# Kernel tuning notes

Hardware: AMD Instinct MI355X
Metric: run time of the kernel (lower is better)

The kernel has to match this reference:

```python
import jax, jax.numpy as jnp
import numpy as np

NUM_EXPERTS = 8
CAP_FACTOR = 1.0
MIN_CAPACITY = 4


def setup_inputs() -> dict:
    key = jax.random.key(0)
    k0, k1, k2, k3 = jax.random.split(key, 4)
    H, F, E = 2048, 8192, NUM_EXPERTS
    hidden_states = jax.random.normal(k0, (4, 2048, H), dtype=jnp.float32)
    wg = jax.random.normal(k1, (H, E), dtype=jnp.float32) * 0.02
    w1 = jax.random.normal(k2, (E, H, F), dtype=jnp.float32) * 0.02
    b1 = jnp.zeros((E, F), dtype=jnp.float32)
    w2 = jax.random.normal(k3, (E, F, H), dtype=jnp.float32) * 0.02
    b2 = jnp.zeros((E, H), dtype=jnp.float32)
    return {"hidden_states": hidden_states, "wg": wg, "w1": w1, "b1": b1,
            "w2": w2, "b2": b2}


def reference(hidden_states, wg, w1, b1, w2, b2):
    E = NUM_EXPERTS
    M = hidden_states.shape[-1]
    x = hidden_states.reshape(-1, M)                     # [S, M] tokens
    S = x.shape[0]
    capacity = max(int(np.ceil(S / E * CAP_FACTOR)), MIN_CAPACITY)  # static

    # --- top-1 gating (DeepSpeed top1gating, fp32) ---
    logits = x.astype(jnp.float32) @ wg                  # [S, E]
    gates = jax.nn.softmax(logits, axis=-1)              # [S, E]
    idx1 = jnp.argmax(gates, axis=1)                     # [S]
    mask1 = jax.nn.one_hot(idx1, E, dtype=jnp.int32)     # [S, E]

    # load-balancing aux loss and per-expert counts
    me = jnp.mean(gates, axis=0)
    ce = jnp.mean(mask1.astype(jnp.float32), axis=0)
    l_aux = jnp.sum(me * ce) * E
    exp_counts = jnp.sum(mask1, axis=0)                  # [E]

    # capacity enforcement (use_rts=False -> keep earliest tokens per expert)
    locations1 = jnp.cumsum(mask1, axis=0) - 1           # [S, E] slot index
    mask1 = mask1 * (locations1 < capacity).astype(jnp.int32)
    mask1f = mask1.astype(gates.dtype)
    gates = gates * mask1f                               # zero dropped/other experts
    locs_s = jnp.sum(locations1 * mask1, axis=1)         # [S] slot of each token
    locs_sc = jax.nn.one_hot(locs_s, capacity, dtype=gates.dtype)  # [S, C]

    # combine / dispatch tensors
    combine = jnp.einsum('se,sc->sec', gates, locs_sc)   # [S, E, C]
    dispatch = (combine > 0).astype(x.dtype)             # bool mask as float

    # dispatch -> grouped expert MLP -> combine
    dispatched = jnp.einsum('sec,sm->ecm', dispatch, x)  # [E, C, M]
    h = jax.nn.gelu(jnp.einsum('ecm,emf->ecf', dispatched, w1) + b1[:, None, :])
    expert_out = jnp.einsum('ecf,efm->ecm', h, w2) + b2[:, None, :]
    out = jnp.einsum('sec,ecm->sm', combine.astype(x.dtype), expert_out)

    return out.reshape(hidden_states.shape), l_aux, exp_counts
```

## Files before the change

### kernel.cpp

```cpp
#include <hip/hip_runtime.h>
#include <stdint.h>

#define E_ 8
#define S_ 8192
#define H_ 2048
#define F_ 8192
#define C_ 1024
#define OUTN (S_*H_)

typedef __bf16 bf16x8 __attribute__((ext_vector_type(8)));
typedef float  f32x4  __attribute__((ext_vector_type(4)));
typedef unsigned short us8 __attribute__((ext_vector_type(8)));

__device__ __forceinline__ unsigned short f2bf(float f) {
    union { float f; unsigned u; } v; v.f = f;
    unsigned r = (v.u + 0x7FFFu + ((v.u >> 16) & 1u)) >> 16;
    return (unsigned short)r;
}

__device__ __forceinline__ void gload16(const void* g, void* l) {
    auto gp = (const __attribute__((address_space(1))) void*)(unsigned long long)(uintptr_t)g;
    auto lp = (__attribute__((address_space(3))) void*)(unsigned int)(uintptr_t)l;
    __builtin_amdgcn_global_load_lds(gp, lp, 16, 0, 0);
}

#define SB() __builtin_amdgcn_sched_barrier(0)
#define BAR() do { SB(); __builtin_amdgcn_s_barrier(); SB(); } while(0)

__global__ void zero_kernel(float* __restrict__ o, int n) {
    int i = blockIdx.x * blockDim.x + threadIdx.x;
    int st = gridDim.x * blockDim.x;
    for (; i < n; i += st) o[i] = 0.f;
}

__global__ __launch_bounds__(256)
void transpose_cvt(const float* __restrict__ src, unsigned short* __restrict__ dst,
                   int R, int Cc)
{
    __shared__ float t[64][65];
    int tilesR = R >> 6, tilesC = Cc >> 6;
    int per_e = tilesR * tilesC;
    int bid = blockIdx.x;
    int e  = bid / per_e;
    int rm = bid - e * per_e;
    int tc = rm / tilesR;
    int tr = rm - tc * tilesR;

    const float* s = src + (size_t)e * R * Cc + (size_t)(tr * 64) * Cc + tc * 64;
    int tid = threadIdx.x;
    int rr = tid >> 4;
    int cc = (tid & 15) << 2;
#pragma unroll
    for (int i = 0; i < 4; i++) {
        float4 v = *(const float4*)(s + (size_t)(rr + i * 16) * Cc + cc);
        t[rr + i * 16][cc + 0] = v.x;
        t[rr + i * 16][cc + 1] = v.y;
        t[rr + i * 16][cc + 2] = v.z;
        t[rr + i * 16][cc + 3] = v.w;
    }
    __syncthreads();
    int nl = tid >> 2;
    int kq = (tid & 3) << 4;
    us8 o0, o1;
#pragma unroll
    for (int i = 0; i < 8; i++) o0[i] = f2bf(t[kq + i][nl]);
#pragma unroll
    for (int i = 0; i < 8; i++) o1[i] = f2bf(t[kq + 8 + i][nl]);
    unsigned short* d = dst + (size_t)e * R * Cc + (size_t)(tc * 64 + nl) * R + tr * 64 + kq;
    *reinterpret_cast<us8*>(d)     = o0;
    *reinterpret_cast<us8*>(d + 8) = o1;
}

__global__ __launch_bounds__(256)
void gating_kernel(const float* __restrict__ x, const float* __restrict__ wg,
                   int* __restrict__ expert_id, float* __restrict__ gate_tok,
                   float* __restrict__ gates_all)
{
    int lane = threadIdx.x & 63;
    int wid  = threadIdx.x >> 6;
    int s = blockIdx.x * 4 + wid;
    const float* xs = x + (size_t)s * H_;
    float p[8];
#pragma unroll
    for (int j = 0; j < 8; j++) p[j] = 0.f;
    for (int h = lane; h < H_; h += 64) {
        float xv = xs[h];
        const float4* w4 = (const float4*)(wg + (size_t)h * 8);
        float4 a = w4[0], b = w4[1];
        p[0] += xv * a.x; p[1] += xv * a.y; p[2] += xv * a.z; p[3] += xv * a.w;
        p[4] += xv * b.x; p[5] += xv * b.y; p[6] += xv * b.z; p[7] += xv * b.w;
    }
#pragma unroll
    for (int off = 32; off; off >>= 1) {
#pragma unroll
        for (int j = 0; j < 8; j++) p[j] += __shfl_xor(p[j], off);
    }
    if (lane == 0) {
        float mx = p[0];
#pragma unroll
        for (int j = 1; j < 8; j++) mx = fmaxf(mx, p[j]);
        float ex[8], sum = 0.f;
#pragma unroll
        for (int j = 0; j < 8; j++) { ex[j] = expf(p[j] - mx); sum += ex[j]; }
        float inv = 1.f / sum;
        int am = 0; float best = p[0];
#pragma unroll
        for (int j = 1; j < 8; j++) if (p[j] > best) { best = p[j]; am = j; }
        expert_id[s] = am;
        gate_tok[s]  = expf(best - mx) * inv;
        float* ga = gates_all + (size_t)s * 8;
#pragma unroll
        for (int j = 0; j < 8; j++) ga[j] = ex[j] * inv;
    }
}

__global__ __launch_bounds__(1024)
void scan_kernel(const int* __restrict__ expert_id,
                 const float* __restrict__ gate_tok,
                 const float* __restrict__ gates_all,
                 int* __restrict__ token_slot,
                 float* __restrict__ gate_slot,
                 float* __restrict__ out_tail)
{
    __shared__ unsigned long long wt0[16], wt1[16];
    __shared__ unsigned long long tot0s, tot1s;
    __shared__ float red[1024 * 8];

    int tid = threadIdx.x;
    for (int i = tid; i < E_ * C_; i += 1024) token_slot[i] = -1;

    int ids[8];
#pragma unroll
    for (int j = 0; j < 8; j++) ids[j] = expert_id[tid * 8 + j];

    unsigned long long c0 = 0, c1 = 0;
#pragma unroll
    for (int j = 0; j < 8; j++) {
        int e = ids[j];
        unsigned long long inc = 1ull << ((e & 3) * 16);
        if (e < 4) c0 += inc; else c1 += inc;
    }
    unsigned long long s0 = c0, s1 = c1;
    int lane = tid & 63, w = tid >> 6;
#pragma unroll
    for (int off = 1; off < 64; off <<= 1) {
        unsigned long long t0 = __shfl_up(s0, off);
        unsigned long long t1 = __shfl_up(s1, off);
        if (lane >= off) { s0 += t0; s1 += t1; }
    }
    if (lane == 63) { wt0[w] = s0; wt1[w] = s1; }
    __syncthreads();
    unsigned long long off0 = 0, off1 = 0;
    for (int i = 0; i < w; i++) { off0 += wt0[i]; off1 += wt1[i]; }
    unsigned long long p0 = off0 + s0 - c0;
    unsigned long long p1 = off1 + s1 - c1;

#pragma unroll
    for (int j = 0; j < 8; j++) {
        int stok = tid * 8 + j;
        int e = ids[j];
        int sh = (e & 3) * 16;
        int slot = (int)(((e < 4 ? p0 : p1) >> sh) & 0xFFFFull);
        if (slot < C_) {
            token_slot[e * C_ + slot] = stok;
            gate_slot[e * C_ + slot]  = gate_tok[stok];
        }
        if (e < 4) p0 += 1ull << sh; else p1 += 1ull << sh;
    }
    if (tid == 1023) { tot0s = off0 + s0; tot1s = off1 + s1; }

    float me[8];
#pragma unroll
    for (int e2 = 0; e2 < 8; e2++) me[e2] = 0.f;
#pragma unroll
    for (int j = 0; j < 8; j++) {
        const float* ga = gates_all + (size_t)(tid * 8 + j) * 8;
#pragma unroll
        for (int e2 = 0; e2 < 8; e2++) me[e2] += ga[e2];
    }
#pragma unroll
    for (int e2 = 0; e2 < 8; e2++) red[tid * 8 + e2] = me[e2];
    __syncthreads();
    for (int st = 512; st > 0; st >>= 1) {
        if (tid < st) {
#pragma unroll
            for (int e2 = 0; e2 < 8; e2++) red[tid * 8 + e2] += red[(tid + st) * 8 + e2];
        }
        __syncthreads();
    }
    if (tid == 0) {
        float laux = 0.f;
#pragma unroll
        for (int e2 = 0; e2 < 8; e2++) {
            unsigned long long tv = (e2 < 4) ? tot0s : tot1s;
            float cnt = (float)((tv >> ((e2 & 3) * 16)) & 0xFFFFull);
            laux += red[e2] * cnt;
            out_tail[1 + e2] = cnt;
        }
        out_tail[0] = laux * (8.f / (8192.f * 8192.f));
    }
}

__global__ __launch_bounds__(256)
void gather_kernel(const float* __restrict__ x, const int* __restrict__ token_slot,
                   unsigned short* __restrict__ disp)
{
    int slot = blockIdx.x;
    int tok = token_slot[slot];
    int t = threadIdx.x;
    us8* d = reinterpret_cast<us8*>(disp + (size_t)slot * H_ + t * 8);
    if (tok < 0) {
        us8 z;
#pragma unroll
        for (int i = 0; i < 8; i++) z[i] = 0;
        *d = z;
        return;
    }
    const float4* s4 = (const float4*)(x + (size_t)tok * H_ + t * 8);
    float4 a = s4[0], b = s4[1];
    us8 o;
    o[0] = f2bf(a.x); o[1] = f2bf(a.y); o[2] = f2bf(a.z); o[3] = f2bf(a.w);
    o[4] = f2bf(b.x); o[5] = f2bf(b.y); o[6] = f2bf(b.z); o[7] = f2bf(b.w);
    *d = o;
}

template<int EPI, int K, int N>
__global__ __launch_bounds__(512, 2)
void gemm8p(const unsigned short* __restrict__ A,
            const unsigned short* __restrict__ B,
            const float* __restrict__ bias,
            unsigned short* __restrict__ hout,
            float* __restrict__ fout,
            const int* __restrict__ token_slot,
            const float* __restrict__ gate_slot,
            int Mt, int Nt)
{
    __shared__ char lds[131072];
    constexpr int KB   = K * 2;
    constexpr int HALF = 128 * KB;
    constexpr int NTI  = K / 64;

    int nwg = gridDim.x;
    int bid = blockIdx.x;
    int cpx = nwg >> 3;
    int wg  = (bid & 7) * cpx + (bid >> 3);
    int per_e = Mt * Nt;
    int e  = wg / per_e;
    int r  = wg - e * per_e;
    int nt = r / Mt;
    int mt = r - nt * Mt;

    int tid  = threadIdx.x;
    int lane = tid & 63;
    int wid  = tid >> 6;
    int wr = wid >> 2, wc = wid & 3;

    const char* Ag = (const char*)(A + ((size_t)e * 1024 + (size_t)mt * 256) * (size_t)K);
    const char* Bg = (const char*)(B + ((size_t)e * N    + (size_t)nt * 256) * (size_t)K);

    int r16s   = (tid >> 2) & 15;
    int scs    = ((tid & 3) * 16) ^ ((r16s & 8) << 2);
    int colblk = (tid >> 6) & 1;
    int rb0    = tid >> 7;
    int off0 = (rb0 * 16 + r16s) * KB + colblk * 64 + scs;
    int off1 = off0 + 64 * KB;
    int widb = wid * 1024;

    int lread = (lane & 15) * 64 + (((lane >> 4) * 16) ^ ((lane & 8) << 2));

    auto STAGE = [&](int ldsbase, const char* srcbase) {
        gload16(srcbase + off0, (char*)&lds[ldsbase + widb]);
        gload16(srcbase + off1, (char*)&lds[ldsbase + 8192 + widb]);
    };

    STAGE(0,         Ag);
    STAGE(16384,     Ag + HALF);
    STAGE(32768,     Bg);
    STAGE(49152,     Bg + HALF);
    STAGE(65536,     Ag + 128);
    STAGE(65536 + 16384, Ag + HALF + 128);
    SB(); asm volatile("s_waitcnt vmcnt(4)" ::: "memory"); SB();
    BAR();

    f32x4 acc[8][4];
    f32x4 zv = {0.f, 0.f, 0.f, 0.f};
#pragma unroll
    for (int i = 0; i < 8; i++)
#pragma unroll
        for (int j = 0; j < 4; j++) acc[i][j] = zv;

    int abase_l = wr * 16384 + lread;
    int bbase_l = 32768 + (wc >> 1) * 16384 + (wc & 1) * 8192 + lread;

    for (int t = 0; t < NTI; ++t) {
        int bb  = (t & 1) << 16;
        int ob  = bb ^ 65536;
        const char* ald = lds + bb + abase_l;
        const char* bld = lds + bb + bbase_l;
        bf16x8 alo[4][2], ahi[4][2], blo[2][2], bhi[2][2];

#pragma unroll
        for (int mi = 0; mi < 4; mi++) {
            alo[mi][0] = *(const bf16x8*)(ald + mi * 2048);
            alo[mi][1] = *(const bf16x8*)(ald + mi * 2048 + 1024);
        }
#pragma unroll
        for (int ni = 0; ni < 2; ni++) {
            blo[ni][0] = *(const bf16x8*)(bld + ni * 2048);
            blo[ni][1] = *(const bf16x8*)(bld + ni * 2048 + 1024);
        }
        if (t + 1 < NTI) STAGE(ob + 32768, Bg + (size_t)(t + 1) * 128);
        BAR();
        __builtin_amdgcn_s_setprio(1);
#pragma unroll
        for (int mi = 0; mi < 4; mi++)
#pragma unroll
            for (int ni = 0; ni < 2; ni++) {
                acc[mi][ni] = __builtin_amdgcn_mfma_f32_16x16x32_bf16(alo[mi][0], blo[ni][0], acc[mi][ni], 0, 0, 0);
                acc[mi][ni] = __builtin_amdgcn_mfma_f32_16x16x32_bf16(alo[mi][1], blo[ni][1], acc[mi][ni], 0, 0, 0);
            }
        __builtin_amdgcn_s_setprio(0);
        BAR();

#pragma unroll
        for (int mi = 0; mi < 4; mi++) {
            ahi[mi][0] = *(const bf16x8*)(ald + 8192 + mi * 2048);
            ahi[mi][1] = *(const bf16x8*)(ald + 8192 + mi * 2048 + 1024);
        }
        if (t + 1 < NTI) STAGE(ob + 49152, Bg + HALF + (size_t)(t + 1) * 128);
        BAR();
        __builtin_amdgcn_s_setprio(1);
#pragma unroll
        for (int mi = 0; mi < 4; mi++)
#pragma unroll
            for (int ni = 0; ni < 2; ni++) {
                acc[mi + 4][ni] = __builtin_amdgcn_mfma_f32_16x16x32_bf16(ahi[mi][0], blo[ni][0], acc[mi + 4][ni], 0, 0, 0);
                acc[mi + 4][ni] = __builtin_amdgcn_mfma_f32_16x16x32_bf16(ahi[mi][1], blo[ni][1], acc[mi + 4][ni], 0, 0, 0);
            }
        __builtin_amdgcn_s_setprio(0);
        BAR();

#pragma unroll
        for (int ni = 0; ni < 2; ni++) {
            bhi[ni][0] = *(const bf16x8*)(bld + 4096 + ni * 2048);
            bhi[ni][1] = *(const bf16x8*)(bld + 4096 + ni * 2048 + 1024);
        }
        if (t + 2 < NTI) STAGE(bb, Ag + (size_t)(t + 2) * 128);
        BAR();
        __builtin_amdgcn_s_setprio(1);
#pragma unroll
        for (int mi = 0; mi < 4; mi++)
#pragma unroll
            for (int ni = 0; ni < 2; ni++) {
                acc[mi + 4][ni + 2] = __builtin_amdgcn_mfma_f32_16x16x32_bf16(ahi[mi][0], bhi[ni][0], acc[mi + 4][ni + 2], 0, 0, 0);
                acc[mi + 4][ni + 2] = __builtin_amdgcn_mfma_f32_16x16x32_bf16(ahi[mi][1], bhi[ni][1], acc[mi + 4][ni + 2], 0, 0, 0);
            }
        __builtin_amdgcn_s_setprio(0);
        BAR();

        if (t + 2 < NTI) STAGE(bb + 16384, Ag + HALF + (size_t)(t + 2) * 128);
        BAR();
        __builtin_amdgcn_s_setprio(1);
#pragma unroll
        for (int mi = 0; mi < 4; mi++)
#pragma unroll
            for (int ni = 0; ni < 2; ni++) {
                acc[mi][ni + 2] = __builtin_amdgcn_mfma_f32_16x16x32_bf16(alo[mi][0], bhi[ni][0], acc[mi][ni + 2], 0, 0, 0);
                acc[mi][ni + 2] = __builtin_amdgcn_mfma_f32_16x16x32_bf16(alo[mi][1], bhi[ni][1], acc[mi][ni + 2], 0, 0, 0);
            }
        __builtin_amdgcn_s_setprio(0);
        if (t + 2 < NTI) { SB(); asm volatile("s_waitcnt vmcnt(4)" ::: "memory"); SB(); }
        else             { SB(); asm volatile("s_waitcnt vmcnt(0)" ::: "memory"); SB(); }
        BAR();
    }

    int rbase = wr * 128 + (lane >> 4) * 4;
    int cbase = wc * 64 + (lane & 15);

    if (EPI == 0) {
        size_t rowg = (size_t)e * C_ + (size_t)mt * 256;
        float bb4[4];
#pragma unroll
        for (int ni = 0; ni < 4; ni++)
            bb4[ni] = bias[(size_t)e * N + nt * 256 + cbase + ni * 16];
#pragma unroll
        for (int mi = 0; mi < 8; mi++) {
#pragma unroll
            for (int rr2 = 0; rr2 < 4; rr2++) {
                int m = rbase + mi * 16 + rr2;
                size_t rb = (rowg + (size_t)m) * (size_t)N + nt * 256 + cbase;
#pragma unroll
                for (int ni = 0; ni < 4; ni++) {
                    float v = acc[mi][ni][rr2] + bb4[ni];
                    float u2 = 1.5957691216057308f * (v + 0.044715f * v * v * v);
                    float gl = v * __frcp_rn(1.f + __expf(-u2));
                    hout[rb + ni * 16] = f2bf(gl);
                }
            }
        }
    } else {
        float bb4[4];
#pragma unroll
        for (int ni = 0; ni < 4; ni++)
            bb4[ni] = bias[(size_t)e * N + nt * 256 + cbase + ni * 16];
#pragma unroll
        for (int mi = 0; mi < 8; mi++) {
#pragma unroll
            for (int rr2 = 0; rr2 < 4; rr2++) {
                int c = mt * 256 + rbase + mi * 16 + rr2;
                int tok = token_slot[e * C_ + c];
                if (tok < 0) continue;
                float g = gate_slot[e * C_ + c];
                size_t rb = (size_t)tok * (size_t)N + nt * 256 + cbase;
#pragma unroll
                for (int ni = 0; ni < 4; ni++) {
                    float v = (acc[mi][ni][rr2] + bb4[ni]) * g;
                    fout[rb + ni * 16] = v;
                }
            }
        }
    }
}

extern "C" void kernel_launch(void* const* d_in, const int* in_sizes, int n_in,
                              void* d_out, int out_size, void* d_ws, size_t ws_size,
                              hipStream_t stream)
{
    const float* x   = (const float*)d_in[0];
    const float* wgp = (const float*)d_in[1];
    const float* w1  = (const float*)d_in[2];
    const float* b1  = (const float*)d_in[3];
    const float* w2  = (const float*)d_in[4];
    const float* b2  = (const float*)d_in[5];
    float* out = (float*)d_out;

    char* ws = (char*)d_ws;
    unsigned short* w1t  = (unsigned short*)(ws);
    unsigned short* w2t  = (unsigned short*)(ws + 268435456ull);
    unsigned short* disp = (unsigned short*)(ws + 536870912ull);
    unsigned short* hbuf = (unsigned short*)(ws + 570425344ull);
    int*   expert_id  = (int*)  (ws + 704643072ull);
    float* gate_tok   = (float*)(ws + 704675840ull);
    float* gates_all  = (float*)(ws + 704708608ull);
    int*   token_slot = (int*)  (ws + 704970752ull);
    float* gate_slot  = (float*)(ws + 705003520ull);

    zero_kernel<<<4096, 256, 0, stream>>>(out, out_size);
    transpose_cvt<<<8 * 32 * 128, 256, 0, stream>>>(w1, w1t, 2048, 8192);
    transpose_cvt<<<8 * 128 * 32, 256, 0, stream>>>(w2, w2t, 8192, 2048);
    gating_kernel<<<2048, 256, 0, stream>>>(x, wgp, expert_id, gate_tok, gates_all);
    scan_kernel<<<1, 1024, 0, stream>>>(expert_id, gate_tok, gates_all, token_slot, gate_slot, out + OUTN);
    gather_kernel<<<8192, 256, 0, stream>>>(x, token_slot, disp);
    gemm8p<0, 2048, 8192><<<1024, 512, 0, stream>>>(disp, w1t, b1, hbuf, nullptr, nullptr, nullptr, 4, 32);
    gemm8p<1, 8192, 2048><<<256, 512, 0, stream>>>(hbuf, w2t, b2, nullptr, out, token_slot, gate_slot, 4, 8);
}
```

Measured before the change: 854.8 us.

## Restructure expert GEMM main loop with register-prefetched LDS reads and fewer barriers

Rewrites the bf16 MFMA GEMM main loop so each K-step stages A and B tiles into a double-buffered LDS layout in one batch. LDS fragments are loaded with inline ds_read_b128 asm and explicit lgkmcnt waits, so reads overlap the preceding MFMA groups. The next tile's fragments are prefetched into registers before the final MFMA block. Barriers drop from eight per iteration to two, cutting synchronisation stalls. This raises register pressure and depends on hand-written wait counts being correct.

```diff
diff --git a/kernel.cpp b/kernel.cpp
--- a/kernel.cpp
+++ b/kernel.cpp
@@ -26,6 +26,10 @@
 
 #define SB() __builtin_amdgcn_sched_barrier(0)
 #define BAR() do { SB(); __builtin_amdgcn_s_barrier(); SB(); } while(0)
+#define DSR(d, a, o) asm volatile("ds_read_b128 %0, %1 offset:" #o : "=v"(d) : "v"(a))
+#define WLGKM(n) do { asm volatile("s_waitcnt lgkmcnt(" #n ")" ::: "memory"); SB(); } while(0)
+#define WVM(n)   do { asm volatile("s_waitcnt vmcnt(" #n ")"   ::: "memory"); SB(); } while(0)
+#define MM(accv, af, bf) accv = __builtin_amdgcn_mfma_f32_16x16x32_bf16(af, bf, accv, 0, 0, 0)
 
 __global__ void zero_kernel(float* __restrict__ o, int n) {
     int i = blockIdx.x * blockDim.x + threadIdx.x;
@@ -226,7 +230,7 @@
 
 template<int EPI, int K, int N>
 __global__ __launch_bounds__(512, 2)
-void gemm8p(const unsigned short* __restrict__ A,
+void gemmra(const unsigned short* __restrict__ A,
             const unsigned short* __restrict__ B,
             const float* __restrict__ bias,
             unsigned short* __restrict__ hout,
@@ -236,9 +240,9 @@
             int Mt, int Nt)
 {
     __shared__ char lds[131072];
-    constexpr int KB   = K * 2;
-    constexpr int HALF = 128 * KB;
-    constexpr int NTI  = K / 64;
+    constexpr int KB  = K * 2;
+    constexpr int QG  = 64 * KB;
+    constexpr int NTI = K / 64;
 
     int nwg = gridDim.x;
     int bid = blockIdx.x;
@@ -263,24 +267,36 @@
     int colblk = (tid >> 6) & 1;
     int rb0    = tid >> 7;
     int off0 = (rb0 * 16 + r16s) * KB + colblk * 64 + scs;
-    int off1 = off0 + 64 * KB;
     int widb = wid * 1024;
 
     int lread = (lane & 15) * 64 + (((lane >> 4) * 16) ^ ((lane & 8) << 2));
 
-    auto STAGE = [&](int ldsbase, const char* srcbase) {
-        gload16(srcbase + off0, (char*)&lds[ldsbase + widb]);
-        gload16(srcbase + off1, (char*)&lds[ldsbase + 8192 + widb]);
+    auto SQ = [&](int dstbyte, const char* src) {
+        gload16(src + off0, (char*)lds + dstbyte + widb);
     };
 
-    STAGE(0,         Ag);
-    STAGE(16384,     Ag + HALF);
-    STAGE(32768,     Bg);
-    STAGE(49152,     Bg + HALF);
-    STAGE(65536,     Ag + 128);
-    STAGE(65536 + 16384, Ag + HALF + 128);
-    SB(); asm volatile("s_waitcnt vmcnt(4)" ::: "memory"); SB();
+#pragma unroll
+    for (int j = 0; j < 4; j++) SQ(j * 8192,          Ag + j * QG);
+#pragma unroll
+    for (int j = 0; j < 4; j++) SQ(65536 + j * 8192,  Bg + j * QG);
+#pragma unroll
+    for (int j = 0; j < 4; j++) SQ(32768 + j * 8192,  Ag + j * QG + 128);
+#pragma unroll
+    for (int j = 0; j < 4; j++) SQ(98304 + j * 8192,  Bg + j * QG + 128);
+    WVM(8);
     BAR();
+
+    unsigned a0 = (unsigned)(uintptr_t)lds + wr * 16384 + lread;
+    unsigned b0 = (unsigned)(uintptr_t)lds + 65536 + (wc >> 1) * 16384 + (wc & 1) * 8192 + lread;
+
+    bf16x8 alo[4][2], ahi[4][2], blo[2][2], bhi[2][2];
+
+    DSR(alo[0][0], a0, 0);    DSR(alo[0][1], a0, 1024);
+    DSR(alo[1][0], a0, 2048); DSR(alo[1][1], a0, 3072);
+    DSR(alo[2][0], a0, 4096); DSR(alo[2][1], a0, 5120);
+    DSR(alo[3][0], a0, 6144); DSR(alo[3][1], a0, 7168);
+    DSR(blo[0][0], b0, 0);    DSR(blo[0][1], b0, 1024);
+    DSR(blo[1][0], b0, 2048); DSR(blo[1][1], b0, 3072);
 
     f32x4 acc[8][4];
     f32x4 zv = {0.f, 0.f, 0.f, 0.f};
@@ -289,89 +305,81 @@
 #pragma unroll
         for (int j = 0; j < 4; j++) acc[i][j] = zv;
 
-    int abase_l = wr * 16384 + lread;
-    int bbase_l = 32768 + (wc >> 1) * 16384 + (wc & 1) * 8192 + lread;
-
     for (int t = 0; t < NTI; ++t) {
-        int bb  = (t & 1) << 16;
-        int ob  = bb ^ 65536;
-        const char* ald = lds + bb + abase_l;
-        const char* bld = lds + bb + bbase_l;
-        bf16x8 alo[4][2], ahi[4][2], blo[2][2], bhi[2][2];
-
-#pragma unroll
-        for (int mi = 0; mi < 4; mi++) {
-            alo[mi][0] = *(const bf16x8*)(ald + mi * 2048);
-            alo[mi][1] = *(const bf16x8*)(ald + mi * 2048 + 1024);
-        }
-#pragma unroll
-        for (int ni = 0; ni < 2; ni++) {
-            blo[ni][0] = *(const bf16x8*)(bld + ni * 2048);
-            blo[ni][1] = *(const bf16x8*)(bld + ni * 2048 + 1024);
-        }
-        if (t + 1 < NTI) STAGE(ob + 32768, Bg + (size_t)(t + 1) * 128);
-        BAR();
+        int bsel = (t & 1) << 15;
+        unsigned av  = a0 + bsel;
+        unsigned bv  = b0 + bsel;
+        unsigned avn = av ^ 32768;
+        unsigned bvn = bv ^ 32768;
+
+        DSR(bhi[0][0], bv, 4096); DSR(bhi[0][1], bv, 5120);
+        DSR(bhi[1][0], bv, 6144); DSR(bhi[1][1], bv, 7168);
+        WLGKM(4);
         __builtin_amdgcn_s_setprio(1);
 #pragma unroll
         for (int mi = 0; mi < 4; mi++)
 #pragma unroll
             for (int ni = 0; ni < 2; ni++) {
-                acc[mi][ni] = __builtin_amdgcn_mfma_f32_16x16x32_bf16(alo[mi][0], blo[ni][0], acc[mi][ni], 0, 0, 0);
-                acc[mi][ni] = __builtin_amdgcn_mfma_f32_16x16x32_bf16(alo[mi][1], blo[ni][1], acc[mi][ni], 0, 0, 0);
+                MM(acc[mi][ni], alo[mi][0], blo[ni][0]);
+                MM(acc[mi][ni], alo[mi][1], blo[ni][1]);
+            }
+        __builtin_amdgcn_s_setprio(0);
+
+        DSR(ahi[0][0], av, 8192);  DSR(ahi[0][1], av, 9216);
+        DSR(ahi[1][0], av, 10240); DSR(ahi[1][1], av, 11264);
+        DSR(ahi[2][0], av, 12288); DSR(ahi[2][1], av, 13312);
+        DSR(ahi[3][0], av, 14336); DSR(ahi[3][1], av, 15360);
+        WLGKM(8);
+        __builtin_amdgcn_s_setprio(1);
+#pragma unroll
+        for (int mi = 0; mi < 4; mi++)
+#pragma unroll
+            for (int ni = 0; ni < 2; ni++) {
+                MM(acc[mi][ni + 2], alo[mi][0], bhi[ni][0]);
+                MM(acc[mi][ni + 2], alo[mi][1], bhi[ni][1]);
+            }
+        __builtin_amdgcn_s_setprio(0);
+
+        WLGKM(0);
+        __builtin_amdgcn_s_setprio(1);
+#pragma unroll
+        for (int mi = 0; mi < 4; mi++)
+#pragma unroll
+            for (int ni = 0; ni < 2; ni++) {
+                MM(acc[mi + 4][ni], ahi[mi][0], blo[ni][0]);
+                MM(acc[mi + 4][ni], ahi[mi][1], blo[ni][1]);
             }
         __builtin_amdgcn_s_setprio(0);
         BAR();
 
-#pragma unroll
-        for (int mi = 0; mi < 4; mi++) {
-            ahi[mi][0] = *(const bf16x8*)(ald + 8192 + mi * 2048);
-            ahi[mi][1] = *(const bf16x8*)(ald + 8192 + mi * 2048 + 1024);
-        }
-        if (t + 1 < NTI) STAGE(ob + 49152, Bg + HALF + (size_t)(t + 1) * 128);
+        if (t + 2 < NTI) {
+            size_t ko = (size_t)(t + 2) * 128;
+#pragma unroll
+            for (int j = 0; j < 4; j++) SQ(bsel + j * 8192,         Ag + j * QG + ko);
+#pragma unroll
+            for (int j = 0; j < 4; j++) SQ(bsel + 65536 + j * 8192, Bg + j * QG + ko);
+            WVM(8);
+        } else {
+            WVM(0);
+        }
         BAR();
+        if (t + 1 < NTI) {
+            DSR(alo[0][0], avn, 0);    DSR(alo[0][1], avn, 1024);
+            DSR(alo[1][0], avn, 2048); DSR(alo[1][1], avn, 3072);
+            DSR(alo[2][0], avn, 4096); DSR(alo[2][1], avn, 5120);
+            DSR(alo[3][0], avn, 6144); DSR(alo[3][1], avn, 7168);
+            DSR(blo[0][0], bvn, 0);    DSR(blo[0][1], bvn, 1024);
+            DSR(blo[1][0], bvn, 2048); DSR(blo[1][1], bvn, 3072);
+        }
         __builtin_amdgcn_s_setprio(1);
 #pragma unroll
         for (int mi = 0; mi < 4; mi++)
 #pragma unroll
             for (int ni = 0; ni < 2; ni++) {
-                acc[mi + 4][ni] = __builtin_amdgcn_mfma_f32_16x16x32_bf16(ahi[mi][0], blo[ni][0], acc[mi + 4][ni], 0, 0, 0);
-                acc[mi + 4][ni] = __builtin_amdgcn_mfma_f32_16x16x32_bf16(ahi[mi][1], blo[ni][1], acc[mi + 4][ni], 0, 0, 0);
+                MM(acc[mi + 4][ni + 2], ahi[mi][0], bhi[ni][0]);
+                MM(acc[mi + 4][ni + 2], ahi[mi][1], bhi[ni][1]);
             }
         __builtin_amdgcn_s_setprio(0);
-        BAR();
-
-#pragma unroll
-        for (int ni = 0; ni < 2; ni++) {
-            bhi[ni][0] = *(const bf16x8*)(bld + 4096 + ni * 2048);
-            bhi[ni][1] = *(const bf16x8*)(bld + 4096 + ni * 2048 + 1024);
-        }
-        if (t + 2 < NTI) STAGE(bb, Ag + (size_t)(t + 2) * 128);
-        BAR();
-        __builtin_amdgcn_s_setprio(1);
-#pragma unroll
-        for (int mi = 0; mi < 4; mi++)
-#pragma unroll
-            for (int ni = 0; ni < 2; ni++) {
-                acc[mi + 4][ni + 2] = __builtin_amdgcn_mfma_f32_16x16x32_bf16(ahi[mi][0], bhi[ni][0], acc[mi + 4][ni + 2], 0, 0, 0);
-                acc[mi + 4][ni + 2] = __builtin_amdgcn_mfma_f32_16x16x32_bf16(ahi[mi][1], bhi[ni][1], acc[mi + 4][ni + 2], 0, 0, 0);
-            }
-        __builtin_amdgcn_s_setprio(0);
-        BAR();
-
-        if (t + 2 < NTI) STAGE(bb + 16384, Ag + HALF + (size_t)(t + 2) * 128);
-        BAR();
-        __builtin_amdgcn_s_setprio(1);
-#pragma unroll
-        for (int mi = 0; mi < 4; mi++)
-#pragma unroll
-            for (int ni = 0; ni < 2; ni++) {
-                acc[mi][ni + 2] = __builtin_amdgcn_mfma_f32_16x16x32_bf16(alo[mi][0], bhi[ni][0], acc[mi][ni + 2], 0, 0, 0);
-                acc[mi][ni + 2] = __builtin_amdgcn_mfma_f32_16x16x32_bf16(alo[mi][1], bhi[ni][1], acc[mi][ni + 2], 0, 0, 0);
-            }
-        __builtin_amdgcn_s_setprio(0);
-        if (t + 2 < NTI) { SB(); asm volatile("s_waitcnt vmcnt(4)" ::: "memory"); SB(); }
-        else             { SB(); asm volatile("s_waitcnt vmcnt(0)" ::: "memory"); SB(); }
-        BAR();
     }
 
     int rbase = wr * 128 + (lane >> 4) * 4;
@@ -451,6 +459,6 @@
     gating_kernel<<<2048, 256, 0, stream>>>(x, wgp, expert_id, gate_tok, gates_all);
     scan_kernel<<<1, 1024, 0, stream>>>(expert_id, gate_tok, gates_all, token_slot, gate_slot, out + OUTN);
     gather_kernel<<<8192, 256, 0, stream>>>(x, token_slot, disp);
-    gemm8p<0, 2048, 8192><<<1024, 512, 0, stream>>>(disp, w1t, b1, hbuf, nullptr, nullptr, nullptr, 4, 32);
-    gemm8p<1, 8192, 2048><<<256, 512, 0, stream>>>(hbuf, w2t, b2, nullptr, out, token_slot, gate_slot, 4, 8);
-}
+    gemmra<0, 2048, 8192><<<1024, 512, 0, stream>>>(disp, w1t, b1, hbuf, nullptr, nullptr, nullptr, 4, 32);
+    gemmra<1, 8192, 2048><<<256, 512, 0, stream>>>(hbuf, w2t, b2, nullptr, out, token_slot, gate_slot, 4, 8);
+}
```

New measurement: 893.6 us. +4.5%, slower.
